# Kernel tuning notes

Hardware: AMD Instinct MI355X
Metric: run time of the kernel (lower is better)

Reference implementation:

```python
import jax, jax.numpy as jnp
import numpy as np

NUM_GROUPS = 32
EPS = 1e-5


def group_norm(x, w, b):
    # x: [B, C, H, W]
    B, C, H, W = x.shape
    xg = x.reshape(B, NUM_GROUPS, C // NUM_GROUPS, H, W)
    mean = jnp.mean(xg, axis=(2, 3, 4), keepdims=True)
    var = jnp.var(xg, axis=(2, 3, 4), keepdims=True)
    xg = (xg - mean) * jax.lax.rsqrt(var + EPS)
    xn = xg.reshape(B, C, H, W)
    return xn * w[None, :, None, None] + b[None, :, None, None]


def conv1x1(x, w, b):
    # x: [B, C, H, W], w: [O, C], b: [O]
    return jnp.einsum('bchw,oc->bohw', x, w) + b[None, :, None, None]


def setup_inputs() -> dict:
    key = jax.random.key(0)
    ks = jax.random.split(key, 10)
    C = 512
    x = jax.random.normal(ks[0], (4, C, 64, 64), dtype=jnp.float32)
    s = 1.0 / np.sqrt(C)
    return {
        'x': x,
        'gn_w': jnp.ones((C,), jnp.float32),
        'gn_b': jnp.zeros((C,), jnp.float32),
        'q_w': jax.random.normal(ks[1], (C, C), jnp.float32) * s,
        'q_b': jax.random.normal(ks[2], (C,), jnp.float32) * 0.01,
        'k_w': jax.random.normal(ks[3], (C, C), jnp.float32) * s,
        'k_b': jax.random.normal(ks[4], (C,), jnp.float32) * 0.01,
        'v_w': jax.random.normal(ks[5], (C, C), jnp.float32) * s,
        'v_b': jax.random.normal(ks[6], (C,), jnp.float32) * 0.01,
        'p_w': jax.random.normal(ks[7], (C, C), jnp.float32) * s,
        'p_b': jax.random.normal(ks[8], (C,), jnp.float32) * 0.01,
    }


def reference(x, gn_w, gn_b, q_w, q_b, k_w, k_b, v_w, v_b, p_w, p_b):
    h_ = group_norm(x, gn_w, gn_b)
    q = conv1x1(h_, q_w, q_b)
    k = conv1x1(h_, k_w, k_b)
    v = conv1x1(h_, v_w, v_b)
    b, c, h, w = q.shape
    n = h * w
    q = q.reshape(b, c, n).transpose(0, 2, 1)   # [b, n, c]
    k = k.reshape(b, c, n)                       # [b, c, n]
    scores = jnp.einsum('bic,bcj->bij', q, k) * (c ** -0.5)  # [b, n, n]
    attn = jax.nn.softmax(scores, axis=-1)
    v = v.reshape(b, c, n)                       # [b, c, n]
    # h_[b,c,i] = sum_j v[b,c,j] * attn[b,i,j]
    h_out = jnp.einsum('bcj,bij->bci', v, attn).reshape(b, c, h, w)
    return x + conv1x1(h_out, p_w, p_b)
```

## Files before the change

kernel.cpp:

```cpp
#include <hip/hip_runtime.h>
#include <hip/hip_bf16.h>
#include <stdint.h>

#define AS1 __attribute__((address_space(1)))
#define AS3 __attribute__((address_space(3)))

typedef unsigned short ushort_t;
typedef __attribute__((ext_vector_type(8))) short short8;
typedef __attribute__((ext_vector_type(4))) float floatx4;
typedef __attribute__((ext_vector_type(16))) float floatx16;
typedef __attribute__((ext_vector_type(2))) unsigned int uint2v;

__device__ __forceinline__ ushort_t f2b(float f) {
    union { float f; unsigned int i; } x; x.f = f;
    unsigned int r = x.i + 0x7fffu + ((x.i >> 16) & 1u);
    return (ushort_t)(r >> 16);
}
__device__ __forceinline__ float b2f(ushort_t u) {
    union { unsigned int i; float f; } x; x.i = ((unsigned int)u) << 16; return x.f;
}
__device__ __forceinline__ void gl2lds16(const void* g, void* l) {
    __builtin_amdgcn_global_load_lds(
        (const AS1 unsigned int*)g,
        (AS3 unsigned int*)l,
        16, 0, 0);
}
__device__ __forceinline__ void plswap(unsigned& a, unsigned& b) {
#if __has_builtin(__builtin_amdgcn_permlane32_swap)
    uint2v r = __builtin_amdgcn_permlane32_swap(a, b, false, false);
    a = r.x; b = r.y;
#else
    asm volatile("v_permlane32_swap_b32 %0, %1" : "+v"(a), "+v"(b));
#endif
}

static constexpr int CCH = 512;
static constexpr int NSP = 4096;
static constexpr int NG  = 32;

__global__ __launch_bounds__(256) void gn_stats(const float* __restrict__ x,
                                                float* __restrict__ mean,
                                                float* __restrict__ rstd) {
    const long base = (long)blockIdx.x * 65536;
    const int t = threadIdx.x;
    float s1 = 0.f, s2 = 0.f;
    for (int i = t * 8; i < 65536; i += 256 * 8) {
        float4 a = *(const float4*)(x + base + i);
        float4 b = *(const float4*)(x + base + i + 4);
        s1 += a.x + a.y + a.z + a.w + b.x + b.y + b.z + b.w;
        s2 += a.x * a.x + a.y * a.y + a.z * a.z + a.w * a.w
            + b.x * b.x + b.y * b.y + b.z * b.z + b.w * b.w;
    }
#pragma unroll
    for (int o = 32; o; o >>= 1) { s1 += __shfl_xor(s1, o, 64); s2 += __shfl_xor(s2, o, 64); }
    __shared__ float r1[4], r2[4];
    const int lane = t & 63, wave = t >> 6;
    if (!lane) { r1[wave] = s1; r2[wave] = s2; }
    __syncthreads();
    if (!t) {
        float S1 = r1[0] + r1[1] + r1[2] + r1[3];
        float S2 = r2[0] + r2[1] + r2[2] + r2[3];
        float mu = S1 * (1.f / 65536.f);
        float var = S2 * (1.f / 65536.f) - mu * mu;
        mean[blockIdx.x] = mu;
        rstd[blockIdx.x] = rsqrtf(var + 1e-5f);
    }
}

__global__ __launch_bounds__(256) void w_to_bf16(const float* __restrict__ q,
                                                 const float* __restrict__ k,
                                                 const float* __restrict__ v,
                                                 const float* __restrict__ p,
                                                 const float* __restrict__ qb,
                                                 ushort_t* __restrict__ out,
                                                 float* __restrict__ sqb) {
    const float scl = 0.044194173824159216f;
    const float* srcs[4] = { q, k, v, p };
    const float* s = srcs[blockIdx.y];
    const float m = (blockIdx.y == 0) ? scl : 1.f;
    const long i = ((long)blockIdx.x * 256 + threadIdx.x) * 4;
    float4 f = *(const float4*)(s + i);
    ushort_t o[4] __attribute__((aligned(8)));
    o[0] = f2b(f.x * m); o[1] = f2b(f.y * m); o[2] = f2b(f.z * m); o[3] = f2b(f.w * m);
    *(ushort4*)(out + (long)blockIdx.y * 262144 + i) = *(ushort4*)o;
    if (blockIdx.y == 0 && blockIdx.x == 0 && threadIdx.x < 128) {
        const int j = threadIdx.x * 4;
        float4 b = *(const float4*)(qb + j);
        sqb[j] = b.x * scl; sqb[j + 1] = b.y * scl; sqb[j + 2] = b.z * scl; sqb[j + 3] = b.w * scl;
    }
}

__global__ __launch_bounds__(256) void norm_transpose(const float* __restrict__ x,
                                                      const float* __restrict__ gw,
                                                      const float* __restrict__ gb,
                                                      const float* __restrict__ mean,
                                                      const float* __restrict__ rstd,
                                                      ushort_t* __restrict__ ht) {
    __shared__ ushort_t tile[64 * 65];
    const int b = blockIdx.z, c0 = blockIdx.y * 64, n0 = blockIdx.x * 64;
    const int t = threadIdx.x;
    const float* xb = x + ((long)b * CCH + c0) * NSP + n0;
#pragma unroll
    for (int p = 0; p < 2; ++p) {
        int li = p * 2048 + t * 8;
        int cl = li >> 6, nl = li & 63;
        int c = c0 + cl, g = c >> 4;
        float mu = mean[b * NG + g], rs = rstd[b * NG + g];
        float w  = gw[c] * rs;
        float bb = gb[c] - mu * w;
        float4 a = *(const float4*)(xb + (long)cl * NSP + nl);
        float4 d = *(const float4*)(xb + (long)cl * NSP + nl + 4);
        float f[8] = { a.x, a.y, a.z, a.w, d.x, d.y, d.z, d.w };
#pragma unroll
        for (int j = 0; j < 8; ++j) tile[cl * 65 + nl + j] = f2b(f[j] * w + bb);
    }
    __syncthreads();
#pragma unroll
    for (int p = 0; p < 2; ++p) {
        int li = p * 2048 + t * 8;
        int nl = li >> 6, cl = li & 63;
        ushort_t v[8] __attribute__((aligned(16)));
#pragma unroll
        for (int j = 0; j < 8; ++j) v[j] = tile[(cl + j) * 65 + nl];
        *(uint4*)(ht + ((long)b * NSP + n0 + nl) * CCH + c0 + cl) = *(uint4*)v;
    }
}

template <int BIAS, int OUTM, int RES>
__global__ __launch_bounds__(256, 2) void gemm_tn(
    const ushort_t* __restrict__ A, int lda, long sA,
    const ushort_t* __restrict__ B, int ldb, long sB,
    void* __restrict__ Cp, int ldc, long sC,
    const float* __restrict__ bias,
    const float* __restrict__ resid, long sR,
    float scale, int K) {
    __shared__ short As[128 * 32];
    __shared__ short Bs[128 * 32];
    const int t = threadIdx.x;
    const int lane = t & 63, wave = t >> 6;
    const long bz = blockIdx.z;
    const int m0 = blockIdx.y * 128, n0 = blockIdx.x * 128;

    const ushort_t* Ab = A + bz * sA + (long)(m0 + (t >> 2)) * lda + (t & 3) * 8;
    const ushort_t* Bb = B + bz * sB + (long)(n0 + (t >> 2)) * ldb + (t & 3) * 8;
    short* la = As + t * 8;
    short* lb = Bs + t * 8;

    const int wm = (wave & 1) * 64, wn = (wave >> 1) * 64;
    const int lm = lane & 15, lk = (lane >> 4) * 8;
    const short* pa = As + (wm + lm) * 32 + lk;
    const short* pb = Bs + (wn + lm) * 32 + lk;

    floatx4 acc[4][4];
#pragma unroll
    for (int i = 0; i < 4; ++i)
#pragma unroll
        for (int j = 0; j < 4; ++j) acc[i][j] = (floatx4){0.f, 0.f, 0.f, 0.f};

    for (int k0 = 0; k0 < K; k0 += 32) {
        __syncthreads();
        gl2lds16(Ab, la);
        gl2lds16(Ab + 64 * (long)lda, la + 64 * 32);
        gl2lds16(Bb, lb);
        gl2lds16(Bb + 64 * (long)ldb, lb + 64 * 32);
        Ab += 32; Bb += 32;
        __builtin_amdgcn_s_waitcnt(0);
        __syncthreads();
        short8 af[4], bfr[4];
#pragma unroll
        for (int i = 0; i < 4; ++i) af[i]  = *(const short8*)(pa + i * 16 * 32);
#pragma unroll
        for (int i = 0; i < 4; ++i) bfr[i] = *(const short8*)(pb + i * 16 * 32);
#pragma unroll
        for (int mi = 0; mi < 4; ++mi)
#pragma unroll
            for (int ni = 0; ni < 4; ++ni)
                acc[mi][ni] = __builtin_amdgcn_mfma_f32_16x16x32_bf16(af[mi], bfr[ni], acc[mi][ni], 0, 0, 0);
    }

    const int row4 = (lane >> 4) * 4;
    const int ncol = lane & 15;
#pragma unroll
    for (int mi = 0; mi < 4; ++mi) {
#pragma unroll
        for (int ni = 0; ni < 4; ++ni) {
            const int n = n0 + wn + ni * 16 + ncol;
            float bn = (BIAS == 2) ? bias[n] : 0.f;
#pragma unroll
            for (int r = 0; r < 4; ++r) {
                const int m = m0 + wm + mi * 16 + row4 + r;
                float v = acc[mi][ni][r] * scale;
                if (BIAS == 1) v += bias[m];
                if (BIAS == 2) v += bn;
                if (RES) v += resid[bz * sR + (long)m * ldc + n];
                if (OUTM == 2) {
                    const long idxv = bz * sC + (long)(n >> 5) * 16384 + (long)((n >> 4) & 1) * 8192
                                    + (m >> 5) * 512 + ((n >> 3) & 1) * 256 + (m & 31) * 8 + (n & 7);
                    ((ushort_t*)Cp)[idxv] = f2b(v);
                } else {
                    const long idx = bz * sC + (long)m * ldc + n;
                    if (OUTM == 1) ((float*)Cp)[idx] = v;
                    else           ((ushort_t*)Cp)[idx] = f2b(v);
                }
            }
        }
    }
}

__global__ __launch_bounds__(256, 1) void flash_attn(const ushort_t* __restrict__ Qt,
                                                     const ushort_t* __restrict__ Kt,
                                                     const ushort_t* __restrict__ Vp,
                                                     ushort_t* __restrict__ pO0,
                                                     ushort_t* __restrict__ pO1,
                                                     float* __restrict__ ml) {
    __shared__ short Klds[2 * 16384];
    const int t = threadIdx.x;
    const int lane = t & 63, wave = t >> 6;
    const int l31 = lane & 31, hi = lane >> 5;
    const int blk = blockIdx.x;
    const int xcd = blk & 7;
    const int bb = xcd >> 1;
    const int split = xcd & 1;
    const int rows0 = (blk >> 3) * 128 + wave * 32;
    const int j_lo = split * 2048;

    const ushort_t* Qb = Qt + ((long)bb * NSP + rows0 + l31) * CCH + hi * 8;
    short8 qf[32];
#pragma unroll
    for (int s = 0; s < 32; ++s) qf[s] = *(const short8*)(Qb + s * 16);

    floatx16 acc[16];
#pragma unroll
    for (int i = 0; i < 16; ++i)
        acc[i] = (floatx16){0.f,0.f,0.f,0.f,0.f,0.f,0.f,0.f,0.f,0.f,0.f,0.f,0.f,0.f,0.f,0.f};
    float lsum = 0.f;

    const ushort_t* KtB = Kt + (long)bb * NSP * CCH;
    const ushort_t* vpb = Vp + (long)bb * NSP * CCH + (long)(j_lo >> 5) * 16384 + lane * 8;

#define STAGE_K(buf, J0)                                                          \
    {                                                                             \
        short* kb_ = Klds + (buf) * 16384;                                        \
        _Pragma("unroll")                                                         \
        for (int i_ = 0; i_ < 8; ++i_) {                                          \
            const int ch_ = i_ * 256 + t;                                         \
            const int jr_ = ch_ >> 6, m_ = ch_ & 63;                              \
            const int ms_ = m_ ^ (jr_ & 15);                                      \
            gl2lds16(KtB + (long)((J0) + jr_) * CCH + ms_ * 8, kb_ + ch_ * 8);    \
        }                                                                         \
    }

    STAGE_K(0, j_lo);
    __builtin_amdgcn_s_waitcnt(0);
    __syncthreads();

    const int exr = (l31 & 15) ^ hi;
    const short* kroot = Klds + l31 * 512;

    int j0 = j_lo;
    for (int tile = 0; tile < 64; ++tile) {
        const int cur = tile & 1;

        short8 vr[8];
#pragma unroll
        for (int u = 0; u < 8; ++u)
            vr[u] = *(const short8*)(vpb + (u >> 1) * 512 + (u & 1) * 8192);

        if (tile + 1 < 64) STAGE_K(cur ^ 1, j0 + 32);

        const short* kp = kroot + cur * 16384;
        floatx16 sE = (floatx16){0.f,0.f,0.f,0.f,0.f,0.f,0.f,0.f,0.f,0.f,0.f,0.f,0.f,0.f,0.f,0.f};
        floatx16 sO = sE;
#pragma unroll
        for (int i = 0; i < 16; ++i) {
            short8 k0 = *(const short8*)(kp + (((4 * i)     ^ exr) << 3));
            short8 k1 = *(const short8*)(kp + (((4 * i + 2) ^ exr) << 3));
            sE = __builtin_amdgcn_mfma_f32_32x32x16_bf16(k0, qf[2 * i],     sE, 0, 0, 0);
            sO = __builtin_amdgcn_mfma_f32_32x32x16_bf16(k1, qf[2 * i + 1], sO, 0, 0, 0);
        }

        float pv_[16];
#pragma unroll
        for (int r = 0; r < 16; ++r) { pv_[r] = __expf(sE[r] + sO[r] - 12.f); lsum += pv_[r]; }
        unsigned pk[8];
#pragma unroll
        for (int g = 0; g < 4; ++g) {
            asm("v_cvt_pk_bf16_f32 %0, %1, %2" : "=v"(pk[2 * g])     : "v"(pv_[4 * g]),     "v"(pv_[4 * g + 1]));
            asm("v_cvt_pk_bf16_f32 %0, %1, %2" : "=v"(pk[2 * g + 1]) : "v"(pv_[4 * g + 2]), "v"(pv_[4 * g + 3]));
        }
        plswap(pk[0], pk[2]);
        plswap(pk[1], pk[3]);
        plswap(pk[4], pk[6]);
        plswap(pk[5], pk[7]);
        union { unsigned u[4]; short8 s8; } uA, uB;
        uA.u[0] = pk[0]; uA.u[1] = pk[1]; uA.u[2] = pk[2]; uA.u[3] = pk[3];
        uB.u[0] = pk[4]; uB.u[1] = pk[5]; uB.u[2] = pk[6]; uB.u[3] = pk[7];
        const short8 PA0 = uA.s8;
        const short8 PA1 = uB.s8;

#pragma unroll
        for (int u = 0; u < 32; ++u) {
            const int i = u >> 1;
            acc[i] = __builtin_amdgcn_mfma_f32_32x32x16_bf16((u & 1) ? PA1 : PA0, vr[u & 7], acc[i], 0, 0, 0);
            if (u < 24)
                vr[u & 7] = *(const short8*)(vpb + ((u + 8) >> 1) * 512 + ((u + 8) & 1) * 8192);
        }

        __builtin_amdgcn_s_waitcnt(0);
        __syncthreads();
        j0 += 32;
        vpb += 16384;
    }
#undef STAGE_K

    const float lt = lsum + __shfl_xor(lsum, 32, 64);
    ushort_t* pOut = (split ? pO1 : pO0) + ((long)bb * NSP + rows0) * CCH;
#pragma unroll
    for (int dt = 0; dt < 16; ++dt)
#pragma unroll
        for (int r = 0; r < 16; ++r) {
            const int rl = (r & 3) + 8 * (r >> 2) + 4 * hi;
            pOut[(long)rl * CCH + dt * 32 + l31] = f2b(acc[dt][r]);
        }
    if (hi == 0) {
        ml[(long)split * 4 * NSP + (long)bb * NSP + rows0 + l31] = lt;
    }
}

__global__ __launch_bounds__(256) void merge_splits(ushort_t* __restrict__ pO0,
                                                    const ushort_t* __restrict__ pO1,
                                                    const float* __restrict__ ml) {
    const long f = ((long)blockIdx.x * 256 + threadIdx.x) * 8;
    const long row = f >> 9;
    const float inv = 1.f / (ml[row] + ml[(long)4 * NSP + row]);
    uint4 u0 = *(const uint4*)(pO0 + f);
    uint4 u1 = *(const uint4*)(pO1 + f);
    const unsigned int* a = (const unsigned int*)&u0;
    const unsigned int* b = (const unsigned int*)&u1;
    ushort_t out[8] __attribute__((aligned(16)));
#pragma unroll
    for (int i = 0; i < 4; ++i) {
        float x0 = __uint_as_float(a[i] << 16), y0 = __uint_as_float(a[i] & 0xffff0000u);
        float x1 = __uint_as_float(b[i] << 16), y1 = __uint_as_float(b[i] & 0xffff0000u);
        out[2 * i]     = f2b((x0 + x1) * inv);
        out[2 * i + 1] = f2b((y0 + y1) * inv);
    }
    *(uint4*)(pO0 + f) = *(uint4*)out;
}

extern "C" void kernel_launch(void* const* d_in, const int* in_sizes, int n_in,
                              void* d_out, int out_size, void* d_ws, size_t ws_size,
                              hipStream_t stream) {
    const float* x   = (const float*)d_in[0];
    const float* gnw = (const float*)d_in[1];
    const float* gnb = (const float*)d_in[2];
    const float* qw  = (const float*)d_in[3];
    const float* qb  = (const float*)d_in[4];
    const float* kw  = (const float*)d_in[5];
    const float* kb  = (const float*)d_in[6];
    const float* vw  = (const float*)d_in[7];
    const float* vb  = (const float*)d_in[8];
    const float* pw  = (const float*)d_in[9];
    const float* pb  = (const float*)d_in[10];
    float* out = (float*)d_out;
    (void)in_sizes; (void)n_in; (void)out_size; (void)ws_size;

    const long E = (long)NSP * CCH;
    char* ws = (char*)d_ws;
    float*    mean = (float*)ws;
    float*    rstd = (float*)(ws + 512);
    ushort_t* wb   = (ushort_t*)(ws + 1024);
    float*    sqb  = (float*)(wb + 4 * 262144);
    float*    ml   = sqb + 512;
    ushort_t* ht   = (ushort_t*)(ml + 2 * 4 * NSP);
    ushort_t* Kt   = ht + 4 * E;
    ushort_t* Vp   = Kt + 4 * E;
    ushort_t* Qt   = Vp + 4 * E;
    ushort_t* hOT  = Qt + 4 * E;
    ushort_t* qwb = wb, *kwb = wb + 262144, *vwb = wb + 2 * 262144, *pwb = wb + 3 * 262144;

    gn_stats<<<128, 256, 0, stream>>>(x, mean, rstd);
    w_to_bf16<<<dim3(256, 4), 256, 0, stream>>>(qw, kw, vw, pw, qb, wb, sqb);
    norm_transpose<<<dim3(64, 8, 4), 256, 0, stream>>>(x, gnw, gnb, mean, rstd, ht);
    gemm_tn<2, 0, 0><<<dim3(4, 32, 4), 256, 0, stream>>>(ht, 512, E, qwb, 512, 0, Qt, 512, E, sqb, nullptr, 0, 1.f, 512);
    gemm_tn<2, 0, 0><<<dim3(4, 32, 4), 256, 0, stream>>>(ht, 512, E, kwb, 512, 0, Kt, 512, E, kb, nullptr, 0, 1.f, 512);
    gemm_tn<1, 2, 0><<<dim3(32, 4, 4), 256, 0, stream>>>(vwb, 512, 0, ht, 512, E, Vp, 4096, E, vb, nullptr, 0, 1.f, 512);
    flash_attn<<<256, 256, 0, stream>>>(Qt, Kt, Vp, hOT, ht, ml);
    merge_splits<<<4096, 256, 0, stream>>>(hOT, ht, ml);
    gemm_tn<1, 1, 1><<<dim3(32, 4, 4), 256, 0, stream>>>(pwb, 512, 0, hOT, 512, E,
                                                         out, 4096, E, pb, x, E, 1.f, 512);
}
```

Measured before the change: 395.5 us.

## Switch flash attention to 16x16x32 MFMA tiles with two blocks per CU

The attention kernel moves from 32x32x16 to 16x16x32 bf16 MFMA. Each wave now handles 16 query rows instead of 32, so the grid doubles to 512 blocks and launch bounds ask for two blocks per CU. The V layout written by the V-projection GEMM and the K staging permutation in LDS are reworked to match the new fragment shapes, which also removes the permlane swap. The goal is more occupancy and latency hiding, paid for with twice as many K tile loads into LDS per query row and smaller, less efficient MFMA shapes.

```diff
diff --git a/kernel.cpp b/kernel.cpp
--- a/kernel.cpp
+++ b/kernel.cpp
@@ -8,8 +8,6 @@
 typedef unsigned short ushort_t;
 typedef __attribute__((ext_vector_type(8))) short short8;
 typedef __attribute__((ext_vector_type(4))) float floatx4;
-typedef __attribute__((ext_vector_type(16))) float floatx16;
-typedef __attribute__((ext_vector_type(2))) unsigned int uint2v;
 
 __device__ __forceinline__ ushort_t f2b(float f) {
     union { float f; unsigned int i; } x; x.f = f;
@@ -24,14 +22,6 @@
         (const AS1 unsigned int*)g,
         (AS3 unsigned int*)l,
         16, 0, 0);
-}
-__device__ __forceinline__ void plswap(unsigned& a, unsigned& b) {
-#if __has_builtin(__builtin_amdgcn_permlane32_swap)
-    uint2v r = __builtin_amdgcn_permlane32_swap(a, b, false, false);
-    a = r.x; b = r.y;
-#else
-    asm volatile("v_permlane32_swap_b32 %0, %1" : "+v"(a), "+v"(b));
-#endif
 }
 
 static constexpr int CCH = 512;
@@ -194,8 +184,8 @@
                 if (BIAS == 2) v += bn;
                 if (RES) v += resid[bz * sR + (long)m * ldc + n];
                 if (OUTM == 2) {
-                    const long idxv = bz * sC + (long)(n >> 5) * 16384 + (long)((n >> 4) & 1) * 8192
-                                    + (m >> 5) * 512 + ((n >> 3) & 1) * 256 + (m & 31) * 8 + (n & 7);
+                    const long idxv = bz * sC + (long)(n >> 5) * 16384 + (long)(m >> 4) * 512
+                                    + (m & 15) * 8 + ((n >> 3) & 3) * 128 + (n & 7);
                     ((ushort_t*)Cp)[idxv] = f2b(v);
                 } else {
                     const long idx = bz * sC + (long)m * ldc + n;
@@ -207,7 +197,7 @@
     }
 }
 
-__global__ __launch_bounds__(256, 1) void flash_attn(const ushort_t* __restrict__ Qt,
+__global__ __launch_bounds__(256, 2) void flash_attn(const ushort_t* __restrict__ Qt,
                                                      const ushort_t* __restrict__ Kt,
                                                      const ushort_t* __restrict__ Vp,
                                                      ushort_t* __restrict__ pO0,
@@ -216,94 +206,85 @@
     __shared__ short Klds[2 * 16384];
     const int t = threadIdx.x;
     const int lane = t & 63, wave = t >> 6;
-    const int l31 = lane & 31, hi = lane >> 5;
+    const int c16 = lane & 15, g = lane >> 4;
     const int blk = blockIdx.x;
     const int xcd = blk & 7;
     const int bb = xcd >> 1;
     const int split = xcd & 1;
-    const int rows0 = (blk >> 3) * 128 + wave * 32;
+    const int rows0 = (blk >> 3) * 64 + wave * 16;
     const int j_lo = split * 2048;
 
-    const ushort_t* Qb = Qt + ((long)bb * NSP + rows0 + l31) * CCH + hi * 8;
-    short8 qf[32];
-#pragma unroll
-    for (int s = 0; s < 32; ++s) qf[s] = *(const short8*)(Qb + s * 16);
-
-    floatx16 acc[16];
-#pragma unroll
-    for (int i = 0; i < 16; ++i)
-        acc[i] = (floatx16){0.f,0.f,0.f,0.f,0.f,0.f,0.f,0.f,0.f,0.f,0.f,0.f,0.f,0.f,0.f,0.f};
+    const ushort_t* Qb = Qt + ((long)bb * NSP + rows0 + c16) * CCH + g * 8;
+    short8 qf[16];
+#pragma unroll
+    for (int kc = 0; kc < 16; ++kc) qf[kc] = *(const short8*)(Qb + kc * 32);
+
+    floatx4 acc[32];
+#pragma unroll
+    for (int i = 0; i < 32; ++i) acc[i] = (floatx4){0.f, 0.f, 0.f, 0.f};
     float lsum = 0.f;
 
     const ushort_t* KtB = Kt + (long)bb * NSP * CCH;
     const ushort_t* vpb = Vp + (long)bb * NSP * CCH + (long)(j_lo >> 5) * 16384 + lane * 8;
 
-#define STAGE_K(buf, J0)                                                          \
-    {                                                                             \
-        short* kb_ = Klds + (buf) * 16384;                                        \
-        _Pragma("unroll")                                                         \
-        for (int i_ = 0; i_ < 8; ++i_) {                                          \
-            const int ch_ = i_ * 256 + t;                                         \
-            const int jr_ = ch_ >> 6, m_ = ch_ & 63;                              \
-            const int ms_ = m_ ^ (jr_ & 15);                                      \
-            gl2lds16(KtB + (long)((J0) + jr_) * CCH + ms_ * 8, kb_ + ch_ * 8);    \
-        }                                                                         \
+#define STAGE_K(buf, J0)                                                           \
+    {                                                                              \
+        short* kb_ = Klds + (buf) * 16384;                                         \
+        _Pragma("unroll")                                                          \
+        for (int i_ = 0; i_ < 8; ++i_) {                                           \
+            const int ch_ = i_ * 256 + t;                                          \
+            const int p_ = ch_ >> 6, m_ = ch_ & 63;                                \
+            const int pj_ = 8 * ((p_ >> 2) & 3) + 4 * (p_ >> 4) + (p_ & 3);        \
+            const int ms_ = m_ ^ (p_ & 15);                                        \
+            gl2lds16(KtB + (long)((J0) + pj_) * CCH + ms_ * 8, kb_ + ch_ * 8);     \
+        }                                                                          \
     }
 
     STAGE_K(0, j_lo);
     __builtin_amdgcn_s_waitcnt(0);
     __syncthreads();
 
-    const int exr = (l31 & 15) ^ hi;
-    const short* kroot = Klds + l31 * 512;
-
     int j0 = j_lo;
     for (int tile = 0; tile < 64; ++tile) {
         const int cur = tile & 1;
 
-        short8 vr[8];
-#pragma unroll
-        for (int u = 0; u < 8; ++u)
-            vr[u] = *(const short8*)(vpb + (u >> 1) * 512 + (u & 1) * 8192);
+        short8 vr[4];
+#pragma unroll
+        for (int u = 0; u < 4; ++u)
+            vr[u] = *(const short8*)(vpb + u * 512);
 
         if (tile + 1 < 64) STAGE_K(cur ^ 1, j0 + 32);
 
-        const short* kp = kroot + cur * 16384;
-        floatx16 sE = (floatx16){0.f,0.f,0.f,0.f,0.f,0.f,0.f,0.f,0.f,0.f,0.f,0.f,0.f,0.f,0.f,0.f};
-        floatx16 sO = sE;
-#pragma unroll
-        for (int i = 0; i < 16; ++i) {
-            short8 k0 = *(const short8*)(kp + (((4 * i)     ^ exr) << 3));
-            short8 k1 = *(const short8*)(kp + (((4 * i + 2) ^ exr) << 3));
-            sE = __builtin_amdgcn_mfma_f32_32x32x16_bf16(k0, qf[2 * i],     sE, 0, 0, 0);
-            sO = __builtin_amdgcn_mfma_f32_32x32x16_bf16(k1, qf[2 * i + 1], sO, 0, 0, 0);
+        const short* kp = Klds + cur * 16384 + (long)c16 * 512;
+        floatx4 sE = (floatx4){0.f, 0.f, 0.f, 0.f};
+        floatx4 sO = sE;
+#pragma unroll
+        for (int kc = 0; kc < 16; ++kc) {
+            const int gr = ((kc * 4 + g) ^ c16) * 8;
+            short8 k0 = *(const short8*)(kp + gr);
+            short8 k1 = *(const short8*)(kp + 8192 + gr);
+            sE = __builtin_amdgcn_mfma_f32_16x16x32_bf16(k0, qf[kc], sE, 0, 0, 0);
+            sO = __builtin_amdgcn_mfma_f32_16x16x32_bf16(k1, qf[kc], sO, 0, 0, 0);
         }
 
-        float pv_[16];
-#pragma unroll
-        for (int r = 0; r < 16; ++r) { pv_[r] = __expf(sE[r] + sO[r] - 12.f); lsum += pv_[r]; }
-        unsigned pk[8];
-#pragma unroll
-        for (int g = 0; g < 4; ++g) {
-            asm("v_cvt_pk_bf16_f32 %0, %1, %2" : "=v"(pk[2 * g])     : "v"(pv_[4 * g]),     "v"(pv_[4 * g + 1]));
-            asm("v_cvt_pk_bf16_f32 %0, %1, %2" : "=v"(pk[2 * g + 1]) : "v"(pv_[4 * g + 2]), "v"(pv_[4 * g + 3]));
-        }
-        plswap(pk[0], pk[2]);
-        plswap(pk[1], pk[3]);
-        plswap(pk[4], pk[6]);
-        plswap(pk[5], pk[7]);
-        union { unsigned u[4]; short8 s8; } uA, uB;
-        uA.u[0] = pk[0]; uA.u[1] = pk[1]; uA.u[2] = pk[2]; uA.u[3] = pk[3];
-        uB.u[0] = pk[4]; uB.u[1] = pk[5]; uB.u[2] = pk[6]; uB.u[3] = pk[7];
-        const short8 PA0 = uA.s8;
-        const short8 PA1 = uB.s8;
-
-#pragma unroll
-        for (int u = 0; u < 32; ++u) {
-            const int i = u >> 1;
-            acc[i] = __builtin_amdgcn_mfma_f32_32x32x16_bf16((u & 1) ? PA1 : PA0, vr[u & 7], acc[i], 0, 0, 0);
-            if (u < 24)
-                vr[u & 7] = *(const short8*)(vpb + ((u + 8) >> 1) * 512 + ((u + 8) & 1) * 8192);
+        float pv_[8];
+#pragma unroll
+        for (int r = 0; r < 4; ++r) { pv_[r] = __expf(sE[r] - 12.f); pv_[4 + r] = __expf(sO[r] - 12.f); }
+#pragma unroll
+        for (int r = 0; r < 8; ++r) lsum += pv_[r];
+        unsigned pk[4];
+#pragma unroll
+        for (int w = 0; w < 4; ++w)
+            asm("v_cvt_pk_bf16_f32 %0, %1, %2" : "=v"(pk[w]) : "v"(pv_[2 * w]), "v"(pv_[2 * w + 1]));
+        union { unsigned u[4]; short8 s8; } uP;
+        uP.u[0] = pk[0]; uP.u[1] = pk[1]; uP.u[2] = pk[2]; uP.u[3] = pk[3];
+        const short8 PA = uP.s8;
+
+#pragma unroll
+        for (int dt = 0; dt < 32; ++dt) {
+            acc[dt] = __builtin_amdgcn_mfma_f32_16x16x32_bf16(PA, vr[dt & 3], acc[dt], 0, 0, 0);
+            if (dt < 28)
+                vr[dt & 3] = *(const short8*)(vpb + (dt + 4) * 512);
         }
 
         __builtin_amdgcn_s_waitcnt(0);
@@ -313,17 +294,16 @@
     }
 #undef STAGE_K
 
-    const float lt = lsum + __shfl_xor(lsum, 32, 64);
+    lsum += __shfl_xor(lsum, 16, 64);
+    lsum += __shfl_xor(lsum, 32, 64);
     ushort_t* pOut = (split ? pO1 : pO0) + ((long)bb * NSP + rows0) * CCH;
 #pragma unroll
-    for (int dt = 0; dt < 16; ++dt)
-#pragma unroll
-        for (int r = 0; r < 16; ++r) {
-            const int rl = (r & 3) + 8 * (r >> 2) + 4 * hi;
-            pOut[(long)rl * CCH + dt * 32 + l31] = f2b(acc[dt][r]);
-        }
-    if (hi == 0) {
-        ml[(long)split * 4 * NSP + (long)bb * NSP + rows0 + l31] = lt;
+    for (int dt = 0; dt < 32; ++dt)
+#pragma unroll
+        for (int r = 0; r < 4; ++r)
+            pOut[(long)(4 * g + r) * CCH + dt * 16 + c16] = f2b(acc[dt][r]);
+    if (g == 0) {
+        ml[(long)split * 4 * NSP + (long)bb * NSP + rows0 + c16] = lsum;
     }
 }
 
@@ -385,7 +365,7 @@
     gemm_tn<2, 0, 0><<<dim3(4, 32, 4), 256, 0, stream>>>(ht, 512, E, qwb, 512, 0, Qt, 512, E, sqb, nullptr, 0, 1.f, 512);
     gemm_tn<2, 0, 0><<<dim3(4, 32, 4), 256, 0, stream>>>(ht, 512, E, kwb, 512, 0, Kt, 512, E, kb, nullptr, 0, 1.f, 512);
     gemm_tn<1, 2, 0><<<dim3(32, 4, 4), 256, 0, stream>>>(vwb, 512, 0, ht, 512, E, Vp, 4096, E, vb, nullptr, 0, 1.f, 512);
-    flash_attn<<<256, 256, 0, stream>>>(Qt, Kt, Vp, hOT, ht, ml);
+    flash_attn<<<512, 256, 0, stream>>>(Qt, Kt, Vp, hOT, ht, ml);
     merge_splits<<<4096, 256, 0, stream>>>(hOT, ht, ml);
     gemm_tn<1, 1, 1><<<dim3(32, 4, 4), 256, 0, stream>>>(pwb, 512, 0, hOT, 512, E,
                                                          out, 4096, E, pb, x, E, 1.f, 512);
```

Result: slower. 791.6 us (+100.1%).
